# Performance work log

Hardware: AMD Instinct MI355X
Metric: run time of the kernel (lower is better)

## Reference

```python
import jax, jax.numpy as jnp
import numpy as np

TEMP = 0.05


def _l2norm(x, axis=-1, eps=1e-12):
    n = jnp.sqrt(jnp.sum(x * x, axis=axis, keepdims=True))
    return x / jnp.maximum(n, eps)


def setup_inputs() -> dict:
    key = jax.random.key(0)
    k1, k2, k3 = jax.random.split(key, 3)
    B, D, N = 1024, 2048, 16384
    inputs = jax.random.normal(k1, (B, D), dtype=jnp.float32)
    targets = jax.random.randint(k2, (B,), 0, N, dtype=jnp.int32).astype(jnp.int64)
    # cluster memory bank: initialized to unit-norm centroids (buffer is zeros in
    # torch but is always filled with normalized centroids before use)
    features = _l2norm(jax.random.normal(k3, (N, D), dtype=jnp.float32))
    return {"inputs": inputs, "targets": targets, "features": features}


def reference(inputs, targets, features):
    # ClusterMemory.forward: normalize -> cosine sim vs bank -> / temp
    xn = _l2norm(inputs, axis=1)            # [B, D]
    out = (xn @ features.T) / TEMP          # [B, N]
    return out
```

## Files before the change

### kernel.cpp

```cpp
#include <hip/hip_runtime.h>
#include <hip/hip_bf16.h>


typedef short bf16x8 __attribute__((ext_vector_type(8)));
typedef float f32x4  __attribute__((ext_vector_type(4)));

#define D_K   2048
#define N_N   16384
#define M_M   1024
#define TEMP_INV 20.0f

__device__ __forceinline__ unsigned short f2bf(float f) {
    unsigned u = __builtin_bit_cast(unsigned, f);
    u += 0x7FFFu + ((u >> 16) & 1u);
    return (unsigned short)(u >> 16);
}

#define GLOAD16(g, l) __builtin_amdgcn_global_load_lds(                        \
    (const __attribute__((address_space(1))) unsigned int*)(g),                \
    (__attribute__((address_space(3))) unsigned int*)(l), 16, 0, 0)

__global__ __launch_bounds__(256) void anorm_kernel(const float* __restrict__ x,
                                                    unsigned short* __restrict__ abf) {
    int row = blockIdx.x;
    int t = threadIdx.x;
    const float4* xr = reinterpret_cast<const float4*>(x + (size_t)row * D_K);
    float4 a = xr[t * 2];
    float4 b = xr[t * 2 + 1];
    float s = a.x*a.x + a.y*a.y + a.z*a.z + a.w*a.w
            + b.x*b.x + b.y*b.y + b.z*b.z + b.w*b.w;
    #pragma unroll
    for (int off = 32; off > 0; off >>= 1) s += __shfl_down(s, off);
    __shared__ float ps[4];
    __shared__ float sbc;
    if ((t & 63) == 0) ps[t >> 6] = s;
    __syncthreads();
    if (t == 0) {
        float tot = ps[0] + ps[1] + ps[2] + ps[3];
        sbc = 1.0f / fmaxf(sqrtf(tot), 1e-12f);
    }
    __syncthreads();
    float rs = sbc;
    bf16x8 v;
    v[0] = (short)f2bf(a.x * rs); v[1] = (short)f2bf(a.y * rs);
    v[2] = (short)f2bf(a.z * rs); v[3] = (short)f2bf(a.w * rs);
    v[4] = (short)f2bf(b.x * rs); v[5] = (short)f2bf(b.y * rs);
    v[6] = (short)f2bf(b.z * rs); v[7] = (short)f2bf(b.w * rs);
    *reinterpret_cast<bf16x8*>(abf + (size_t)row * D_K + t * 8) = v;
}

__global__ __launch_bounds__(256) void bconv_kernel(const float* __restrict__ B,
                                                    unsigned short* __restrict__ bbf) {
    const size_t nv = (size_t)N_N * D_K / 8;
    size_t stride = (size_t)gridDim.x * blockDim.x;
    for (size_t v = (size_t)blockIdx.x * blockDim.x + threadIdx.x; v < nv; v += stride) {
        const float4* p = reinterpret_cast<const float4*>(B) + v * 2;
        float4 a = p[0], b = p[1];
        bf16x8 o;
        o[0] = (short)f2bf(a.x); o[1] = (short)f2bf(a.y);
        o[2] = (short)f2bf(a.z); o[3] = (short)f2bf(a.w);
        o[4] = (short)f2bf(b.x); o[5] = (short)f2bf(b.y);
        o[6] = (short)f2bf(b.z); o[7] = (short)f2bf(b.w);
        reinterpret_cast<bf16x8*>(bbf)[v] = o;
    }
}

__global__ __launch_bounds__(512, 2) void gemm8_kernel(const unsigned short* __restrict__ Abf,
                                                       const unsigned short* __restrict__ Bbf,
                                                       float* __restrict__ C) {
    __shared__ __align__(16) unsigned short lds[65536];

    int bid = blockIdx.x;
    int wg  = (bid & 7) * 32 + (bid >> 3);
    int tm  = wg & 3, tn = wg >> 2;
    int m_blk = tm * 256, n_blk = tn * 256;

    int t = threadIdx.x, lane = t & 63, w = t >> 6;
    int wm = w >> 2, wn = w & 3;

    int l15  = lane & 15;
    int slot = ((lane >> 4) ^ ((l15 >> 1) & 3)) * 16;
    int aoff = (wm * 128 + l15) * 64 + slot;
    int boff = (wn * 64  + l15) * 64 + slot;

    const unsigned short* gA[2];
    const unsigned short* gB[2];
    int sdst[2];
    #pragma unroll
    for (int pass = 0; pass < 2; ++pass) {
        int r = pass * 128 + (t >> 2);
        int csrc = (t & 3) ^ ((r >> 1) & 3);
        gA[pass] = Abf + (size_t)(m_blk + r) * D_K + csrc * 8;
        gB[pass] = Bbf + (size_t)(n_blk + r) * D_K + csrc * 8;
        sdst[pass] = pass * 8192 + w * 1024;
    }

    auto stage = [&](int mat, int s, int b, int ktile) {
        int kt = ktile < 32 ? ktile : 31;
        int koff = kt * 64 + s * 32;
        int ldsb = b * 65536 + mat * 32768 + s * 16384;
        GLOAD16((mat ? gB[0] : gA[0]) + koff, (char*)lds + ldsb + sdst[0]);
        GLOAD16((mat ? gB[1] : gA[1]) + koff, (char*)lds + ldsb + sdst[1]);
    };

    f32x4 acc[8][4] = {};
    bf16x8 bfr[4];

#define PHASE(b, mh, s, LOADB, stMat, stS, stB, stKt, VM)                      \
    {                                                                          \
        bf16x8 af[4];                                                          \
        _Pragma("unroll")                                                      \
        for (int f = 0; f < 4; ++f)                                            \
            af[f] = *reinterpret_cast<const bf16x8*>(                          \
                (char*)lds + (b) * 65536 + (s) * 16384 + aoff +                \
                ((mh) * 64 + f * 16) * 64);                                    \
        if (LOADB) {                                                           \
            _Pragma("unroll")                                                  \
            for (int n = 0; n < 4; ++n)                                        \
                bfr[n] = *reinterpret_cast<const bf16x8*>(                     \
                    (char*)lds + (b) * 65536 + 32768 + (s) * 16384 + boff +    \
                    n * 1024);                                                 \
        }                                                                      \
        stage(stMat, stS, stB, stKt);                                          \
        asm volatile("s_barrier" ::: "memory");                                \
        asm volatile("s_waitcnt lgkmcnt(0)" ::: "memory");                     \
        __builtin_amdgcn_sched_barrier(0);                                     \
        __builtin_amdgcn_s_setprio(1);                                         \
        _Pragma("unroll")                                                      \
        for (int f = 0; f < 4; ++f) {                                          \
            _Pragma("unroll")                                                  \
            for (int n = 0; n < 4; ++n)                                        \
                acc[(mh) * 4 + f][n] = __builtin_amdgcn_mfma_f32_16x16x32_bf16(\
                    af[f], bfr[n], acc[(mh) * 4 + f][n], 0, 0, 0);             \
        }                                                                      \
        __builtin_amdgcn_s_setprio(0);                                         \
        if (VM) asm volatile("s_waitcnt vmcnt(8)" ::: "memory");               \
        asm volatile("s_barrier" ::: "memory");                                \
    }

    stage(0, 0, 0, 0);
    stage(1, 0, 0, 0);
    stage(0, 1, 0, 0);
    stage(1, 1, 0, 0);
    stage(0, 0, 1, 1);
    stage(1, 0, 1, 1);
    asm volatile("s_waitcnt vmcnt(8)" ::: "memory");
    asm volatile("s_barrier" ::: "memory");

    for (int u = 0; u < 16; ++u) {
        int t1 = 2 * u + 1;
        PHASE(0, 0, 0, true,  0, 1, 1, t1,     false)
        PHASE(0, 1, 0, false, 1, 1, 1, t1,     true )
        PHASE(0, 0, 1, true,  0, 0, 0, t1 + 1, false)
        PHASE(0, 1, 1, false, 1, 0, 0, t1 + 1, true )
        PHASE(1, 0, 0, true,  0, 1, 0, t1 + 1, false)
        PHASE(1, 1, 0, false, 1, 1, 0, t1 + 1, true )
        PHASE(1, 0, 1, true,  0, 0, 1, t1 + 2, false)
        PHASE(1, 1, 1, false, 1, 0, 1, t1 + 2, true )
    }
#undef PHASE

    #pragma unroll
    for (int f = 0; f < 8; ++f) {
        int r = m_blk + wm * 128 + (f >> 2) * 64 + (f & 3) * 16 + (lane >> 4) * 4;
        #pragma unroll
        for (int j = 0; j < 4; ++j) {
            float* cp = C + (size_t)(r + j) * N_N + n_blk + wn * 64 + (lane & 15);
            #pragma unroll
            for (int n = 0; n < 4; ++n)
                cp[n * 16] = acc[f][n][j] * TEMP_INV;
        }
    }
}

__global__ __launch_bounds__(256) void rnorm_kernel(const float* __restrict__ x,
                                                    float* __restrict__ rn) {
    int row = blockIdx.x;
    const float4* xr = reinterpret_cast<const float4*>(x + (size_t)row * D_K);
    int t = threadIdx.x;
    float4 a = xr[t];
    float4 b = xr[t + 256];
    float s = a.x*a.x + a.y*a.y + a.z*a.z + a.w*a.w
            + b.x*b.x + b.y*b.y + b.z*b.z + b.w*b.w;
    #pragma unroll
    for (int off = 32; off > 0; off >>= 1) s += __shfl_down(s, off);
    __shared__ float ps[4];
    int wave = t >> 6, lane = t & 63;
    if (lane == 0) ps[wave] = s;
    __syncthreads();
    if (t == 0) {
        float tot = ps[0] + ps[1] + ps[2] + ps[3];
        rn[row] = 1.0f / fmaxf(sqrtf(tot), 1e-12f);
    }
}

__global__ __launch_bounds__(256, 2) void gemm_kernel(const float* __restrict__ A,
                                                      const float* __restrict__ Bm,
                                                      const float* __restrict__ rn,
                                                      float* __restrict__ C) {
    constexpr int BK = 64;
    __shared__ __align__(16) short lAs[128 * BK];
    __shared__ __align__(16) short lBs[128 * BK];
    int bid = blockIdx.x;
    int nb  = (bid & 7) * 128 + (bid >> 3);
    int tm  = nb & 7;
    int tn  = nb >> 3;
    int m0 = tm * 128, n0 = tn * 128;
    int t = threadIdx.x;
    int lane = t & 63, w = t >> 6;
    int wr = (w >> 1) * 64, wc = (w & 1) * 64;
    f32x4 acc[4][4] = {};
    float4 ra[4][2], rb[4][2];
    float  sc[4];
    int    srow[4], sgrp[4];
    #pragma unroll
    for (int i = 0; i < 4; ++i) {
        int li = t + i * 256;
        srow[i] = li >> 3;
        sgrp[i] = li & 7;
        sc[i]   = rn[m0 + srow[i]];
    }
    auto load_tiles = [&](int kt) {
        int k0 = kt * BK;
        #pragma unroll
        for (int i = 0; i < 4; ++i) {
            const float4* pa = reinterpret_cast<const float4*>(
                A + (size_t)(m0 + srow[i]) * D_K + k0 + sgrp[i] * 8);
            ra[i][0] = pa[0]; ra[i][1] = pa[1];
            const float4* pb = reinterpret_cast<const float4*>(
                Bm + (size_t)(n0 + srow[i]) * D_K + k0 + sgrp[i] * 8);
            rb[i][0] = pb[0]; rb[i][1] = pb[1];
        }
    };
    auto write_tiles = [&]() {
        #pragma unroll
        for (int i = 0; i < 4; ++i) {
            int row = srow[i];
            int slot = sgrp[i] ^ (row & 7);
            float s = sc[i];
            bf16x8 va, vb;
            va[0] = (short)f2bf(ra[i][0].x * s); va[1] = (short)f2bf(ra[i][0].y * s);
            va[2] = (short)f2bf(ra[i][0].z * s); va[3] = (short)f2bf(ra[i][0].w * s);
            va[4] = (short)f2bf(ra[i][1].x * s); va[5] = (short)f2bf(ra[i][1].y * s);
            va[6] = (short)f2bf(ra[i][1].z * s); va[7] = (short)f2bf(ra[i][1].w * s);
            vb[0] = (short)f2bf(rb[i][0].x); vb[1] = (short)f2bf(rb[i][0].y);
            vb[2] = (short)f2bf(rb[i][0].z); vb[3] = (short)f2bf(rb[i][0].w);
            vb[4] = (short)f2bf(rb[i][1].x); vb[5] = (short)f2bf(rb[i][1].y);
            vb[6] = (short)f2bf(rb[i][1].z); vb[7] = (short)f2bf(rb[i][1].w);
            *reinterpret_cast<bf16x8*>(&lAs[row * BK + slot * 8]) = va;
            *reinterpret_cast<bf16x8*>(&lBs[row * BK + slot * 8]) = vb;
        }
    };
    auto compute = [&]() {
        #pragma unroll
        for (int ks = 0; ks < 2; ++ks) {
            bf16x8 af[4], bfr[4];
            #pragma unroll
            for (int f = 0; f < 4; ++f) {
                int arow = wr + f * 16 + (lane & 15);
                int aslot = (ks * 4 + (lane >> 4)) ^ (arow & 7);
                af[f] = *reinterpret_cast<const bf16x8*>(&lAs[arow * BK + aslot * 8]);
                int brow = wc + f * 16 + (lane & 15);
                int bslot = (ks * 4 + (lane >> 4)) ^ (brow & 7);
                bfr[f] = *reinterpret_cast<const bf16x8*>(&lBs[brow * BK + bslot * 8]);
            }
            #pragma unroll
            for (int m = 0; m < 4; ++m)
                #pragma unroll
                for (int n = 0; n < 4; ++n)
                    acc[m][n] = __builtin_amdgcn_mfma_f32_16x16x32_bf16(
                        af[m], bfr[n], acc[m][n], 0, 0, 0);
        }
    };
    load_tiles(0);
    write_tiles();
    for (int kt = 1; kt < D_K / BK; ++kt) {
        __syncthreads();
        load_tiles(kt);
        compute();
        __syncthreads();
        write_tiles();
    }
    __syncthreads();
    compute();
    #pragma unroll
    for (int m = 0; m < 4; ++m) {
        int r = m0 + wr + m * 16 + (lane >> 4) * 4;
        #pragma unroll
        for (int j = 0; j < 4; ++j) {
            float* cp = C + (size_t)(r + j) * N_N + n0 + wc + (lane & 15);
            #pragma unroll
            for (int n = 0; n < 4; ++n)
                cp[n * 16] = acc[m][n][j] * TEMP_INV;
        }
    }
}

extern "C" void kernel_launch(void* const* d_in, const int* in_sizes, int n_in,
                              void* d_out, int out_size, void* d_ws, size_t ws_size,
                              hipStream_t stream) {
    const float* inputs   = (const float*)d_in[0];
    const float* features = (const float*)d_in[2];
    float* out = (float*)d_out;

    const size_t needA = (size_t)M_M * D_K * 2;
    const size_t needB = (size_t)N_N * D_K * 2;
    if (ws_size >= needA + needB) {
        unsigned short* Abf = (unsigned short*)d_ws;
        unsigned short* Bbf = Abf + (size_t)M_M * D_K;
        anorm_kernel<<<M_M, 256, 0, stream>>>(inputs, Abf);
        bconv_kernel<<<2048, 256, 0, stream>>>(features, Bbf);
        gemm8_kernel<<<(M_M / 256) * (N_N / 256), 512, 0, stream>>>(Abf, Bbf, out);
    } else {
        float* rn = (float*)d_ws;
        rnorm_kernel<<<M_M, 256, 0, stream>>>(inputs, rn);
        gemm_kernel<<<(M_M / 128) * (N_N / 128), 256, 0, stream>>>(inputs, features, rn, out);
    }
}
```

Before: 108.0 us.

## Fuse fp32-to-bf16 conversion of feature bank into GEMM B-tile staging

Removes the separate bconv pass that converted the whole fp32 feature bank to bf16 in workspace. The GEMM now loads fp32 B tiles through registers, converts them to bf16 and writes them swizzled into LDS, interleaved with the existing A global-to-LDS loads and new vmcnt waits. This removes a full write and re-read of the bf16 bank and one kernel launch. In exchange, each B tile is read as fp32 (twice the bytes) by every M-tile block, and the kernel carries extra register pressure and conversion ALU work.

```diff
diff --git a/kernel.cpp b/kernel.cpp
--- a/kernel.cpp
+++ b/kernel.cpp
@@ -49,25 +49,9 @@
     *reinterpret_cast<bf16x8*>(abf + (size_t)row * D_K + t * 8) = v;
 }
 
-__global__ __launch_bounds__(256) void bconv_kernel(const float* __restrict__ B,
-                                                    unsigned short* __restrict__ bbf) {
-    const size_t nv = (size_t)N_N * D_K / 8;
-    size_t stride = (size_t)gridDim.x * blockDim.x;
-    for (size_t v = (size_t)blockIdx.x * blockDim.x + threadIdx.x; v < nv; v += stride) {
-        const float4* p = reinterpret_cast<const float4*>(B) + v * 2;
-        float4 a = p[0], b = p[1];
-        bf16x8 o;
-        o[0] = (short)f2bf(a.x); o[1] = (short)f2bf(a.y);
-        o[2] = (short)f2bf(a.z); o[3] = (short)f2bf(a.w);
-        o[4] = (short)f2bf(b.x); o[5] = (short)f2bf(b.y);
-        o[6] = (short)f2bf(b.z); o[7] = (short)f2bf(b.w);
-        reinterpret_cast<bf16x8*>(bbf)[v] = o;
-    }
-}
-
-__global__ __launch_bounds__(512, 2) void gemm8_kernel(const unsigned short* __restrict__ Abf,
-                                                       const unsigned short* __restrict__ Bbf,
-                                                       float* __restrict__ C) {
+__global__ __launch_bounds__(512, 2) void gemm8f_kernel(const unsigned short* __restrict__ Abf,
+                                                        const float* __restrict__ Bm,
+                                                        float* __restrict__ C) {
     __shared__ __align__(16) unsigned short lds[65536];
 
     int bid = blockIdx.x;
@@ -84,29 +68,56 @@
     int boff = (wn * 64  + l15) * 64 + slot;
 
     const unsigned short* gA[2];
-    const unsigned short* gB[2];
     int sdst[2];
     #pragma unroll
     for (int pass = 0; pass < 2; ++pass) {
         int r = pass * 128 + (t >> 2);
         int csrc = (t & 3) ^ ((r >> 1) & 3);
         gA[pass] = Abf + (size_t)(m_blk + r) * D_K + csrc * 8;
-        gB[pass] = Bbf + (size_t)(n_blk + r) * D_K + csrc * 8;
         sdst[pass] = pass * 8192 + w * 1024;
     }
-
-    auto stage = [&](int mat, int s, int b, int ktile) {
+    auto stageA = [&](int s, int b, int ktile) {
         int kt = ktile < 32 ? ktile : 31;
         int koff = kt * 64 + s * 32;
-        int ldsb = b * 65536 + mat * 32768 + s * 16384;
-        GLOAD16((mat ? gB[0] : gA[0]) + koff, (char*)lds + ldsb + sdst[0]);
-        GLOAD16((mat ? gB[1] : gA[1]) + koff, (char*)lds + ldsb + sdst[1]);
+        int ldsb = b * 65536 + s * 16384;
+        GLOAD16(gA[0] + koff, (char*)lds + ldsb + sdst[0]);
+        GLOAD16(gA[1] + koff, (char*)lds + ldsb + sdst[1]);
+    };
+
+    int brow = t >> 1, bhalf = t & 1;
+    const float* gBsrc = Bm + (size_t)(n_blk + brow) * D_K + bhalf * 32;
+    unsigned wbase = (unsigned)(32768 + bhalf * 16384 + brow * 64);
+    int wsw = (brow >> 1) & 3;
+    float4 rB[8];
+    auto loadB = [&](int ktile) {
+        int kt = ktile < 32 ? ktile : 31;
+        const float4* p = reinterpret_cast<const float4*>(gBsrc + kt * 64);
+        #pragma unroll
+        for (int g = 0; g < 8; ++g) rB[g] = p[g];
+    };
+    auto writeB = [&](int b) {
+        char* dst = (char*)lds + b * 65536 + wbase;
+        #pragma unroll
+        for (int g = 0; g < 4; ++g) {
+            float4 x = rB[g * 2], y = rB[g * 2 + 1];
+            bf16x8 v;
+            v[0] = (short)f2bf(x.x); v[1] = (short)f2bf(x.y);
+            v[2] = (short)f2bf(x.z); v[3] = (short)f2bf(x.w);
+            v[4] = (short)f2bf(y.x); v[5] = (short)f2bf(y.y);
+            v[6] = (short)f2bf(y.z); v[7] = (short)f2bf(y.w);
+            *reinterpret_cast<bf16x8*>(dst + ((g ^ wsw) * 16)) = v;
+        }
+    };
+    auto vm12 = [&] { asm volatile("s_waitcnt vmcnt(12)" ::: "memory"); };
+    auto p4w  = [&](int b) {
+        asm volatile("s_waitcnt vmcnt(4)" ::: "memory");
+        writeB(b);
     };
 
     f32x4 acc[8][4] = {};
     bf16x8 bfr[4];
 
-#define PHASE(b, mh, s, LOADB, stMat, stS, stB, stKt, VM)                      \
+#define PHASE(b, mh, s, LOADB, PRE, POST)                                      \
     {                                                                          \
         bf16x8 af[4];                                                          \
         _Pragma("unroll")                                                      \
@@ -121,7 +132,7 @@
                     (char*)lds + (b) * 65536 + 32768 + (s) * 16384 + boff +    \
                     n * 1024);                                                 \
         }                                                                      \
-        stage(stMat, stS, stB, stKt);                                          \
+        PRE;                                                                   \
         asm volatile("s_barrier" ::: "memory");                                \
         asm volatile("s_waitcnt lgkmcnt(0)" ::: "memory");                     \
         __builtin_amdgcn_sched_barrier(0);                                     \
@@ -134,29 +145,30 @@
                     af[f], bfr[n], acc[(mh) * 4 + f][n], 0, 0, 0);             \
         }                                                                      \
         __builtin_amdgcn_s_setprio(0);                                         \
-        if (VM) asm volatile("s_waitcnt vmcnt(8)" ::: "memory");               \
+        POST;                                                                  \
         asm volatile("s_barrier" ::: "memory");                                \
     }
 
-    stage(0, 0, 0, 0);
-    stage(1, 0, 0, 0);
-    stage(0, 1, 0, 0);
-    stage(1, 1, 0, 0);
-    stage(0, 0, 1, 1);
-    stage(1, 0, 1, 1);
-    asm volatile("s_waitcnt vmcnt(8)" ::: "memory");
+    loadB(0);
+    writeB(0);
+    loadB(1);
+    writeB(1);
+    stageA(0, 0, 0);
+    stageA(1, 0, 0);
+    stageA(0, 1, 1);
+    asm volatile("s_waitcnt vmcnt(4)" ::: "memory");
+    asm volatile("s_waitcnt lgkmcnt(0)" ::: "memory");
     asm volatile("s_barrier" ::: "memory");
 
     for (int u = 0; u < 16; ++u) {
-        int t1 = 2 * u + 1;
-        PHASE(0, 0, 0, true,  0, 1, 1, t1,     false)
-        PHASE(0, 1, 0, false, 1, 1, 1, t1,     true )
-        PHASE(0, 0, 1, true,  0, 0, 0, t1 + 1, false)
-        PHASE(0, 1, 1, false, 1, 0, 0, t1 + 1, true )
-        PHASE(1, 0, 0, true,  0, 1, 0, t1 + 1, false)
-        PHASE(1, 1, 0, false, 1, 1, 0, t1 + 1, true )
-        PHASE(1, 0, 1, true,  0, 0, 1, t1 + 2, false)
-        PHASE(1, 1, 1, false, 1, 0, 1, t1 + 2, true )
+        PHASE(0, 0, 0, true,  (loadB(2 * u + 2)),      (void)0)
+        PHASE(0, 1, 0, false, (stageA(1, 1, 2 * u + 1)), (vm12()))
+        PHASE(0, 0, 1, true,  (stageA(0, 0, 2 * u + 2)), (void)0)
+        PHASE(0, 1, 1, false, (void)0,                 (p4w(0)))
+        PHASE(1, 0, 0, true,  (loadB(2 * u + 3)),      (void)0)
+        PHASE(1, 1, 0, false, (stageA(1, 0, 2 * u + 2)), (vm12()))
+        PHASE(1, 0, 1, true,  (stageA(0, 1, 2 * u + 3)), (void)0)
+        PHASE(1, 1, 1, false, (void)0,                 (p4w(1)))
     }
 #undef PHASE
 
@@ -304,13 +316,10 @@
     float* out = (float*)d_out;
 
     const size_t needA = (size_t)M_M * D_K * 2;
-    const size_t needB = (size_t)N_N * D_K * 2;
-    if (ws_size >= needA + needB) {
+    if (ws_size >= needA) {
         unsigned short* Abf = (unsigned short*)d_ws;
-        unsigned short* Bbf = Abf + (size_t)M_M * D_K;
         anorm_kernel<<<M_M, 256, 0, stream>>>(inputs, Abf);
-        bconv_kernel<<<2048, 256, 0, stream>>>(features, Bbf);
-        gemm8_kernel<<<(M_M / 256) * (N_N / 256), 512, 0, stream>>>(Abf, Bbf, out);
+        gemm8f_kernel<<<(M_M / 256) * (N_N / 256), 512, 0, stream>>>(Abf, features, out);
     } else {
         float* rn = (float*)d_ws;
         rnorm_kernel<<<M_M, 256, 0, stream>>>(inputs, rn);
```

After: 135.2 us. 25.1% more time.
